# Performance work log

Hardware: AMD Instinct MI355X
Metric: run time of the kernel (lower is better)

Reference implementation:

```python
import jax, jax.numpy as jnp
import numpy as np

M, N, RANK = 4096, 4096, 64
LORA_ALPHA = 0.8
CODEBOOK_SCALE = 1.03  # E8P12 opt_scale; decompressed weights are divided by it


def fwht(x):
    """Normalized fast Walsh-Hadamard transform along the last axis (power-of-2 length).
    Matches matmul_hadU for power-of-2 dims (had_K is None, K=1)."""
    n = x.shape[-1]
    orig = x.shape
    x = x.reshape(-1, n)
    h = 1
    while h < n:
        x = x.reshape(-1, n // (2 * h), 2, h)
        a, b = x[:, :, 0, :], x[:, :, 1, :]
        x = jnp.stack([a + b, a - b], axis=2).reshape(-1, n)
        h *= 2
    return (x / jnp.sqrt(jnp.float32(n))).reshape(orig)


def decode_e8p(codes, grid):
    """E8P lattice codebook dequant (decompress_packed_e8p semantics).
    codes: int32 [M, N//8], one 16-bit codeword per 8-weight group.
    grid:  int32 [256] packed abs codebook; 8 nibbles per entry, nibble = 2*|w| in {1,3,5,7}.
    Bit layout: [0:8]=abs grid index, [8:15]=signs of first 7 coords,
    [15]=global +/-0.25 shift. 8th sign keeps the negative-sign count even."""
    abs_idx = codes & 0xFF
    sign_bits = (codes >> 8) & 0x7F
    shift_bit = (codes >> 15) & 1
    packed = grid[abs_idx]                                      # [M, N//8] int32
    nibs = (packed[..., None] >> (4 * jnp.arange(8))) & 0xF     # [M, N//8, 8]
    s7 = 1.0 - 2.0 * ((sign_bits[..., None] >> jnp.arange(7)) & 1).astype(jnp.float32)
    s8 = jnp.prod(s7, axis=-1, keepdims=True)                   # parity sign for 8th coord
    signs = jnp.concatenate([s7, s8], axis=-1)                  # [M, N//8, 8]
    delta = (2.0 * shift_bit.astype(jnp.float32) - 1.0)[..., None] * 0.25
    w = signs * (0.5 * nibs.astype(jnp.float32)) + delta
    return w.reshape(codes.shape[0], -1) / CODEBOOK_SCALE       # [M, N]


def build_W(Qidxs, grid, SU, SV, Wscale):
    W = decode_e8p(Qidxs, grid)   # [M, N]
    W = fwht(W)                   # Hadamard over in_features
    W = fwht(W.T).T               # Hadamard over out_features
    # per-channel sign/scale rescale; SV absorbs the global Wscale (SV *= Wscale)
    return W * (SV * Wscale)[:, None] * SU[None, :]


def setup_inputs() -> dict:
    key = jax.random.key(0)
    k1, k2, k3, k4, k5 = jax.random.split(key, 5)
    rng = np.random.default_rng(0)
    # packed abs codebook: 8 nibbles per int32, nibble = 2*|w| in {1,3,5,7}
    nibs = rng.integers(0, 4, size=(256, 8)).astype(np.int64) * 2 + 1
    grid = (nibs * (1 << (4 * np.arange(8)))).sum(axis=1).astype(np.int32)
    # one random 16-bit codeword per 8-weight group (int64 packing pre-split to int32)
    codes = rng.integers(0, 2 ** 16, size=(M, N // 8)).astype(np.int32)
    return {
        "input": jax.random.normal(k1, (1, 1024, N), dtype=jnp.float32),
        "SU": jnp.where(jax.random.uniform(k2, (N,)) < 0.5, -1.0, 1.0).astype(jnp.float32),
        "SV": jnp.where(jax.random.uniform(k3, (M,)) < 0.5, -1.0, 1.0).astype(jnp.float32),
        "Wscale": jnp.float32(0.02),
        "lora_A": jax.random.normal(k4, (M, RANK), dtype=jnp.float32) * 0.01,
        "lora_B": jax.random.normal(k5, (RANK, N), dtype=jnp.float32) * 0.01,
        "Qidxs": jnp.asarray(codes),
        "grid": jnp.asarray(grid),
    }


def reference(input, SU, SV, Wscale, lora_A, lora_B, Qidxs, grid):
    W = build_W(Qidxs, grid, SU, SV, Wscale)            # [M, N] dequantized weight
    out = jnp.einsum("bsn,mn->bsm", input, W)           # base quantized matmul
    lr = jnp.einsum("bsn,rn->bsr", input, lora_B)       # low-rank path
    out = out + LORA_ALPHA * jnp.einsum("bsr,mr->bsm", lr, lora_A)
    return out
```

## Files before the change

### kernel.cpp

```cpp
#include <hip/hip_runtime.h>
#include <hip/hip_bf16.h>

typedef unsigned short u16;
typedef float  floatx4 __attribute__((ext_vector_type(4)));
typedef short  bf16x8  __attribute__((ext_vector_type(8)));

#define GK 4224

__device__ __forceinline__ u16 f2bf_rne(float f) {
  union { float f; unsigned int u; } v; v.f = f;
  unsigned int r = v.u + 0x7FFFu + ((v.u >> 16) & 1u);
  return (u16)(r >> 16);
}

__device__ __forceinline__ void fwht4096_regs(float v[16], float* X, int w, int l) {
#pragma unroll
  for (int h = 1; h < 64; h <<= 1) {
#pragma unroll
    for (int k = 0; k < 16; ++k) {
      float o = __shfl_xor(v[k], h, 64);
      v[k] = (l & h) ? (o - v[k]) : (v[k] + o);
    }
  }
#pragma unroll
  for (int k = 0; k < 16; ++k) X[(w * 16 + k) * 64 + l] = v[k];
  __syncthreads();
  float s4 = (w & 1) ? -1.f : 1.f;
  float s5 = (w & 2) ? -1.f : 1.f;
#pragma unroll
  for (int k = 0; k < 16; ++k) {
    float x00 = X[(k     ) * 64 + l];
    float x01 = X[(k + 16) * 64 + l];
    float x10 = X[(k + 32) * 64 + l];
    float x11 = X[(k + 48) * 64 + l];
    v[k] = (x00 + s4 * x01) + s5 * (x10 + s4 * x11);
  }
#pragma unroll
  for (int h = 1; h < 16; h <<= 1) {
#pragma unroll
    for (int k = 0; k < 16; ++k) {
      if (!(k & h)) { float a = v[k], b = v[k ^ h]; v[k] = a + b; v[k ^ h] = a - b; }
    }
  }
}

__global__ void decode_kernel(const int* __restrict__ codes,
                              const int* __restrict__ grid,
                              u16* __restrict__ Wd) {
  __shared__ int sgrid[256];
  int t = threadIdx.x;
  sgrid[t] = grid[t & 255];
  __syncthreads();
  int idx = blockIdx.x * 256 + t;
  int c = codes[idx];
  int abs_idx   = c & 255;
  int sign_bits = (c >> 8) & 127;
  int dlt       = 2 * ((c >> 15) & 1) - 1;
  int packed    = sgrid[abs_idx];
  int par       = __popc(sign_bits) & 1;
  u16 w[8];
#pragma unroll
  for (int j = 0; j < 8; ++j) {
    int nib = (packed >> (4 * j)) & 15;
    int neg = (j < 7) ? ((sign_bits >> j) & 1) : par;
    int val = (neg ? -2 * nib : 2 * nib) + dlt;
    w[j] = f2bf_rne((float)val);
  }
  uint4 pk;
  pk.x = (unsigned)w[0] | ((unsigned)w[1] << 16);
  pk.y = (unsigned)w[2] | ((unsigned)w[3] << 16);
  pk.z = (unsigned)w[4] | ((unsigned)w[5] << 16);
  pk.w = (unsigned)w[6] | ((unsigned)w[7] << 16);
  int m = idx >> 9, g = idx & 511;
  ((uint4*)Wd)[(size_t)m * (GK / 8) + g] = pk;
}

__global__ __launch_bounds__(256) void prep_A_kernel(const float* __restrict__ loraA,
                                                     const float* __restrict__ SV,
                                                     const float* __restrict__ WscaleP,
                                                     u16* __restrict__ At) {
  __shared__ float X[4096];
  int r = blockIdx.x, t = threadIdx.x, l = t & 63, w = t >> 6;
  float v[16];
#pragma unroll
  for (int k = 0; k < 16; ++k) {
    int i = (w * 16 + k) * 64 + l;
    v[k] = loraA[(size_t)i * 64 + r] * SV[i];
  }
  fwht4096_regs(v, X, w, l);
  float factor = (0.8f * 263.68f / 4096.0f) / WscaleP[0];
#pragma unroll
  for (int k = 0; k < 16; ++k) {
    int i = (w * 16 + k) * 64 + l;
    At[(size_t)r * 4096 + i] = f2bf_rne(v[k] * factor);
  }
}

__global__ void transA_kernel(const u16* __restrict__ At, u16* __restrict__ Wd) {
  __shared__ u16 T[64][65];
  int m0 = blockIdx.x * 64, t = threadIdx.x;
  int c = t & 63, q = t >> 6;
#pragma unroll
  for (int j = 0; j < 16; ++j) {
    int r = q * 16 + j;
    T[r][c] = At[(size_t)r * 4096 + m0 + c];
  }
  __syncthreads();
#pragma unroll
  for (int j = 0; j < 16; ++j) {
    int m = q * 16 + j;
    Wd[(size_t)(m0 + m) * GK + 4096 + c] = T[c][m];
    Wd[(size_t)(m0 + m) * GK + 4160 + c] = 0;
  }
}

__global__ __launch_bounds__(256) void prep_B_kernel(const float* __restrict__ loraB,
                                                     const float* __restrict__ SU,
                                                     u16* __restrict__ Bh) {
  __shared__ float X[4096];
  int r = blockIdx.x, t = threadIdx.x, l = t & 63, w = t >> 6;
  float v[16];
#pragma unroll
  for (int k = 0; k < 16; ++k) {
    int i = (w * 16 + k) * 64 + l;
    v[k] = loraB[(size_t)r * 4096 + i] * SU[i];
  }
  fwht4096_regs(v, X, w, l);
#pragma unroll
  for (int k = 0; k < 16; ++k) {
    int i = (w * 16 + k) * 64 + l;
    Bh[(size_t)r * 4096 + i] = f2bf_rne(v[k] * 0.015625f);
  }
}

__global__ __launch_bounds__(256) void fwht_u_kernel(const float* __restrict__ x,
                                                     const float* __restrict__ SU,
                                                     u16* __restrict__ u) {
  __shared__ float X[4096];
  int s = blockIdx.x, t = threadIdx.x, l = t & 63, w = t >> 6;
  const float* xr = x + (size_t)s * 4096;
  float v[16];
#pragma unroll
  for (int k = 0; k < 16; ++k) {
    int i = (w * 16 + k) * 64 + l;
    v[k] = xr[i] * SU[i];
  }
  fwht4096_regs(v, X, w, l);
  u16* ur = u + (size_t)s * GK;
#pragma unroll
  for (int k = 0; k < 16; ++k) {
    int i = (w * 16 + k) * 64 + l;
    ur[i] = f2bf_rne(v[k] * 0.015625f);
  }
}

__device__ __forceinline__ void stage64(const u16* __restrict__ src, int rowBase,
                                        int kt, char* ldsBase, int wg, int l) {
#pragma unroll
  for (int it = 0; it < 4; ++it) {
    int ci  = it * 4 + wg;
    int row = ci * 8 + (l >> 3);
    int cg  = (l & 7) ^ ((l >> 3) & 7);
    const u16* gp = src + (size_t)(rowBase + row) * GK + kt + cg * 8;
    __builtin_amdgcn_global_load_lds(
        (const __attribute__((address_space(1))) void*)gp,
        (__attribute__((address_space(3))) void*)(ldsBase + ci * 1024), 16, 0, 0);
  }
}

__device__ __forceinline__ void stage64n(const u16* __restrict__ src,
                                         int kt, char* ldsBase, int wg, int l) {
#pragma unroll
  for (int it = 0; it < 2; ++it) {
    int ci  = it * 4 + wg;
    int row = ci * 8 + (l >> 3);
    int cg  = (l & 7) ^ ((l >> 3) & 7);
    const u16* gp = src + (size_t)row * 4096 + kt + cg * 8;
    __builtin_amdgcn_global_load_lds(
        (const __attribute__((address_space(1))) void*)gp,
        (__attribute__((address_space(3))) void*)(ldsBase + ci * 1024), 16, 0, 0);
  }
}

__global__ __launch_bounds__(256) void lr_gemm_kernel(
    const u16* __restrict__ U,
    const u16* __restrict__ Bh,
    float* __restrict__ P) {
  __shared__ char lds[49152];
  int t = threadIdx.x, w = t >> 6, l = t & 63;
  int s0 = blockIdx.x * 128, k0 = blockIdx.y * 1024;
  int lr16 = l & 15, lk = l >> 4;
  char* ldsA = lds;
  char* ldsB = lds + 32768;

  floatx4 acc[2][4];
#pragma unroll
  for (int i = 0; i < 2; ++i)
#pragma unroll
    for (int j = 0; j < 4; ++j) acc[i][j] = (floatx4){0.f, 0.f, 0.f, 0.f};

  const int NT = 16;
  stage64 (U,  s0, k0,      ldsA,         w, l);
  stage64n(Bh,     k0,      ldsB,         w, l);
  stage64 (U,  s0, k0 + 64, ldsA + 16384, w, l);
  stage64n(Bh,     k0 + 64, ldsB + 8192,  w, l);
  asm volatile("s_waitcnt vmcnt(6)" ::: "memory");
  __builtin_amdgcn_s_barrier();

  for (int i = 0; i < NT; ++i) {
    int buf = i & 1;
    const char* sAc = ldsA + buf * 16384;
    const char* sBc = ldsB + buf * 8192;
    bf16x8 a[2][2], b[4][2];
#pragma unroll
    for (int ii = 0; ii < 2; ++ii)
#pragma unroll
      for (int ks = 0; ks < 2; ++ks) {
        int row = w * 32 + ii * 16 + lr16;
        int kb  = ks * 64 + lk * 16;
        a[ii][ks] = *(const bf16x8*)(sAc + (row << 7) + (kb ^ ((row & 7) << 4)));
      }
#pragma unroll
    for (int jj = 0; jj < 4; ++jj)
#pragma unroll
      for (int ks = 0; ks < 2; ++ks) {
        int row = jj * 16 + lr16;
        int kb  = ks * 64 + lk * 16;
        b[jj][ks] = *(const bf16x8*)(sBc + (row << 7) + (kb ^ ((row & 7) << 4)));
      }
    asm volatile("s_waitcnt lgkmcnt(0)" ::: "memory");
    __builtin_amdgcn_sched_barrier(0);
    bool do_stage = (i + 2) < NT;
    if (do_stage) {
      __builtin_amdgcn_s_barrier();
      stage64 (U,  s0, k0 + (i + 2) * 64, ldsA + buf * 16384, w, l);
      stage64n(Bh,     k0 + (i + 2) * 64, ldsB + buf * 8192,  w, l);
    }
#pragma unroll
    for (int ks = 0; ks < 2; ++ks)
#pragma unroll
      for (int ii = 0; ii < 2; ++ii)
#pragma unroll
        for (int jj = 0; jj < 4; ++jj)
          acc[ii][jj] = __builtin_amdgcn_mfma_f32_16x16x32_bf16(
              a[ii][ks], b[jj][ks], acc[ii][jj], 0, 0, 0);
    if (i + 1 < NT) {
      if (do_stage) asm volatile("s_waitcnt vmcnt(6)" ::: "memory");
      else          asm volatile("s_waitcnt vmcnt(0)" ::: "memory");
      __builtin_amdgcn_s_barrier();
    }
  }
  float* Pb = P + (size_t)blockIdx.y * 65536;
#pragma unroll
  for (int ii = 0; ii < 2; ++ii)
#pragma unroll
    for (int jj = 0; jj < 4; ++jj) {
      int col  = jj * 16 + lr16;
      int rowb = s0 + w * 32 + ii * 16 + lk * 4;
#pragma unroll
      for (int q = 0; q < 4; ++q)
        Pb[(size_t)(rowb + q) * 64 + col] = acc[ii][jj][q];
    }
}

__global__ void lr_reduce_kernel(const float* __restrict__ P, u16* __restrict__ u) {
  int idx = blockIdx.x * 256 + threadIdx.x;
  float s = P[idx] + P[65536 + idx] + P[131072 + idx] + P[196608 + idx];
  int ss = idx >> 6, rr = idx & 63;
  u[(size_t)ss * GK + 4096 + rr] = f2bf_rne(s);
  u[(size_t)ss * GK + 4160 + rr] = 0;
}

__global__ __launch_bounds__(512) void gemm_kernel(
    const u16* __restrict__ A,
    const u16* __restrict__ B,
    float* __restrict__ Z) {
  __shared__ char lds[131072];
  int t = threadIdx.x, w = t >> 6, l = t & 63;
  int g = w >> 2, wg = w & 3;
  int m0 = blockIdx.x * 128, s0 = blockIdx.y * 128;
  int wm = wg >> 1, wn = wg & 1;
  int lr16 = l & 15, lk = l >> 4;
  char* gl = lds + g * 65536;

  floatx4 acc[4][4];
#pragma unroll
  for (int i = 0; i < 4; ++i)
#pragma unroll
    for (int j = 0; j < 4; ++j) acc[i][j] = (floatx4){0.f, 0.f, 0.f, 0.f};

  const int NT2 = 33;
  int kb0 = g * 2112;

  stage64(A, s0, kb0,      gl,         wg, l);
  stage64(B, m0, kb0,      gl + 32768, wg, l);
  stage64(A, s0, kb0 + 64, gl + 16384, wg, l);
  stage64(B, m0, kb0 + 64, gl + 49152, wg, l);
  asm volatile("s_waitcnt vmcnt(8)" ::: "memory");
  __builtin_amdgcn_s_barrier();

  for (int i = 0; i < NT2; ++i) {
    int buf = i & 1;
    const char* sAc = gl + buf * 16384;
    const char* sBc = gl + 32768 + buf * 16384;
    bf16x8 a[4][2], b[4][2];
#pragma unroll
    for (int ii = 0; ii < 4; ++ii)
#pragma unroll
      for (int ks = 0; ks < 2; ++ks) {
        int row = wm * 64 + ii * 16 + lr16;
        int kb  = ks * 64 + lk * 16;
        a[ii][ks] = *(const bf16x8*)(sAc + (row << 7) + (kb ^ ((row & 7) << 4)));
      }
#pragma unroll
    for (int jj = 0; jj < 4; ++jj)
#pragma unroll
      for (int ks = 0; ks < 2; ++ks) {
        int row = wn * 64 + jj * 16 + lr16;
        int kb  = ks * 64 + lk * 16;
        b[jj][ks] = *(const bf16x8*)(sBc + (row << 7) + (kb ^ ((row & 7) << 4)));
      }
    asm volatile("s_waitcnt lgkmcnt(0)" ::: "memory");
    __builtin_amdgcn_sched_barrier(0);
    bool do_stage = (i + 2) < NT2;
    if (do_stage) {
      __builtin_amdgcn_s_barrier();
      stage64(A, s0, kb0 + (i + 2) * 64, gl + buf * 16384, wg, l);
      stage64(B, m0, kb0 + (i + 2) * 64, gl + 32768 + buf * 16384, wg, l);
    }
#pragma unroll
    for (int ks = 0; ks < 2; ++ks)
#pragma unroll
      for (int ii = 0; ii < 4; ++ii)
#pragma unroll
        for (int jj = 0; jj < 4; ++jj)
          acc[ii][jj] = __builtin_amdgcn_mfma_f32_16x16x32_bf16(
              a[ii][ks], b[jj][ks], acc[ii][jj], 0, 0, 0);
    if (i + 1 < NT2) {
      if (do_stage) asm volatile("s_waitcnt vmcnt(8)" ::: "memory");
      else          asm volatile("s_waitcnt vmcnt(0)" ::: "memory");
      __builtin_amdgcn_s_barrier();
    }
  }

  __syncthreads();
  if (g == 1) {
#pragma unroll
    for (int ii = 0; ii < 4; ++ii)
#pragma unroll
      for (int jj = 0; jj < 4; ++jj)
        *(floatx4*)(lds + wg * 16384 + (ii * 4 + jj) * 1024 + l * 16) = acc[ii][jj];
  }
  __syncthreads();
  if (g == 0) {
#pragma unroll
    for (int ii = 0; ii < 4; ++ii)
#pragma unroll
      for (int jj = 0; jj < 4; ++jj) {
        floatx4 o = *(const floatx4*)(lds + wg * 16384 + (ii * 4 + jj) * 1024 + l * 16);
        acc[ii][jj] += o;
        int col  = m0 + wn * 64 + jj * 16 + lr16;
        int rowb = s0 + wm * 64 + ii * 16 + lk * 4;
#pragma unroll
        for (int q = 0; q < 4; ++q)
          Z[(size_t)(rowb + q) * 4096 + col] = acc[ii][jj][q];
      }
  }
}

__global__ __launch_bounds__(256) void final_kernel(const float* __restrict__ SV,
                                                    const float* __restrict__ WscaleP,
                                                    float* __restrict__ out) {
  __shared__ float X[4096];
  int s = blockIdx.x, t = threadIdx.x, l = t & 63, w = t >> 6;
  float* zr = out + (size_t)s * 4096;
  float v[16];
#pragma unroll
  for (int k = 0; k < 16; ++k) v[k] = zr[(w * 16 + k) * 64 + l];
  fwht4096_regs(v, X, w, l);
  float gscale = WscaleP[0] * (1.0f / 263.68f);
#pragma unroll
  for (int k = 0; k < 16; ++k) {
    int i = (w * 16 + k) * 64 + l;
    zr[i] = v[k] * gscale * SV[i];
  }
}

extern "C" void kernel_launch(void* const* d_in, const int* in_sizes, int n_in,
                              void* d_out, int out_size, void* d_ws, size_t ws_size,
                              hipStream_t stream) {
  const float* x      = (const float*)d_in[0];
  const float* SU     = (const float*)d_in[1];
  const float* SV     = (const float*)d_in[2];
  const float* Wscale = (const float*)d_in[3];
  const float* loraA  = (const float*)d_in[4];
  const float* loraB  = (const float*)d_in[5];
  const int*   Qidxs  = (const int*)d_in[6];
  const int*   grid   = (const int*)d_in[7];
  float* out = (float*)d_out;

  char* ws = (char*)d_ws;
  u16* Wd = (u16*)ws;
  u16* u  = (u16*)(ws + 34603008);
  u16* At = (u16*)(ws + 34603008 + 8650752);
  u16* Bh = At;
  float* P = (float*)(ws + 34603008 + 8650752 + 524288);
  float* z = out;

  decode_kernel<<<8192, 256, 0, stream>>>(Qidxs, grid, Wd);
  prep_A_kernel<<<64, 256, 0, stream>>>(loraA, SV, Wscale, At);
  transA_kernel<<<64, 256, 0, stream>>>(At, Wd);
  prep_B_kernel<<<64, 256, 0, stream>>>(loraB, SU, Bh);
  fwht_u_kernel<<<1024, 256, 0, stream>>>(x, SU, u);
  dim3 lg(8, 4);
  lr_gemm_kernel<<<lg, 256, 0, stream>>>(u, Bh, P);
  lr_reduce_kernel<<<256, 256, 0, stream>>>(P, u);
  dim3 gg(32, 8);
  gemm_kernel<<<gg, 512, 0, stream>>>(u, Wd, z);
  final_kernel<<<1024, 256, 0, stream>>>(SV, Wscale, out);
}
```

Measured before the change: 95.46 us.

## Split GEMM K across blocks with bf16 partials reduced in final kernel

The GEMM no longer splits K between two 4-wave groups inside one 512-thread block with an LDS reduction. It now launches a z-dimension of 2 blocks of 256 threads, and each block writes its K-half partial as bf16 into the output buffer. The final FWHT kernel sums the two bf16 partials before the transform. The main loop is also reordered to issue the first-half MFMAs before the barrier and staging, to overlap with loads. This gives more, smaller blocks with half the LDS and removes the in-block reduction, at the cost of bf16 rounding of the partial sums.

```diff
diff --git a/kernel.cpp b/kernel.cpp
--- a/kernel.cpp
+++ b/kernel.cpp
@@ -11,6 +11,10 @@
   union { float f; unsigned int u; } v; v.f = f;
   unsigned int r = v.u + 0x7FFFu + ((v.u >> 16) & 1u);
   return (u16)(r >> 16);
+}
+__device__ __forceinline__ float bf2f(u16 h) {
+  union { unsigned int u; float f; } v; v.u = ((unsigned int)h) << 16;
+  return v.f;
 }
 
 __device__ __forceinline__ void fwht4096_regs(float v[16], float* X, int w, int l) {
@@ -271,17 +275,15 @@
   u[(size_t)ss * GK + 4160 + rr] = 0;
 }
 
-__global__ __launch_bounds__(512) void gemm_kernel(
+__global__ __launch_bounds__(256) void gemm_kernel(
     const u16* __restrict__ A,
     const u16* __restrict__ B,
-    float* __restrict__ Z) {
-  __shared__ char lds[131072];
+    u16* __restrict__ zP) {
+  __shared__ char lds[65536];
   int t = threadIdx.x, w = t >> 6, l = t & 63;
-  int g = w >> 2, wg = w & 3;
-  int m0 = blockIdx.x * 128, s0 = blockIdx.y * 128;
-  int wm = wg >> 1, wn = wg & 1;
+  int m0 = blockIdx.x * 128, s0 = blockIdx.y * 128, g = blockIdx.z;
+  int wm = w >> 1, wn = w & 1;
   int lr16 = l & 15, lk = l >> 4;
-  char* gl = lds + g * 65536;
 
   floatx4 acc[4][4];
 #pragma unroll
@@ -289,83 +291,76 @@
 #pragma unroll
     for (int j = 0; j < 4; ++j) acc[i][j] = (floatx4){0.f, 0.f, 0.f, 0.f};
 
-  const int NT2 = 33;
+  const int NT = 33;
   int kb0 = g * 2112;
 
-  stage64(A, s0, kb0,      gl,         wg, l);
-  stage64(B, m0, kb0,      gl + 32768, wg, l);
-  stage64(A, s0, kb0 + 64, gl + 16384, wg, l);
-  stage64(B, m0, kb0 + 64, gl + 49152, wg, l);
+  stage64(A, s0, kb0,      lds,         w, l);
+  stage64(B, m0, kb0,      lds + 32768, w, l);
+  stage64(A, s0, kb0 + 64, lds + 16384, w, l);
+  stage64(B, m0, kb0 + 64, lds + 49152, w, l);
   asm volatile("s_waitcnt vmcnt(8)" ::: "memory");
   __builtin_amdgcn_s_barrier();
 
-  for (int i = 0; i < NT2; ++i) {
+  for (int i = 0; i < NT; ++i) {
     int buf = i & 1;
-    const char* sAc = gl + buf * 16384;
-    const char* sBc = gl + 32768 + buf * 16384;
+    const char* sAc = lds + buf * 16384;
+    const char* sBc = lds + 32768 + buf * 16384;
     bf16x8 a[4][2], b[4][2];
 #pragma unroll
+    for (int ii = 0; ii < 4; ++ii) {
+      int row = wm * 64 + ii * 16 + lr16;
+      a[ii][0] = *(const bf16x8*)(sAc + (row << 7) + ((lk * 16) ^ ((row & 7) << 4)));
+    }
+#pragma unroll
+    for (int jj = 0; jj < 4; ++jj) {
+      int row = wn * 64 + jj * 16 + lr16;
+      b[jj][0] = *(const bf16x8*)(sBc + (row << 7) + ((lk * 16) ^ ((row & 7) << 4)));
+    }
+#pragma unroll
+    for (int ii = 0; ii < 4; ++ii) {
+      int row = wm * 64 + ii * 16 + lr16;
+      a[ii][1] = *(const bf16x8*)(sAc + (row << 7) + ((64 + lk * 16) ^ ((row & 7) << 4)));
+    }
+#pragma unroll
+    for (int jj = 0; jj < 4; ++jj) {
+      int row = wn * 64 + jj * 16 + lr16;
+      b[jj][1] = *(const bf16x8*)(sBc + (row << 7) + ((64 + lk * 16) ^ ((row & 7) << 4)));
+    }
+#pragma unroll
     for (int ii = 0; ii < 4; ++ii)
 #pragma unroll
-      for (int ks = 0; ks < 2; ++ks) {
-        int row = wm * 64 + ii * 16 + lr16;
-        int kb  = ks * 64 + lk * 16;
-        a[ii][ks] = *(const bf16x8*)(sAc + (row << 7) + (kb ^ ((row & 7) << 4)));
-      }
-#pragma unroll
-    for (int jj = 0; jj < 4; ++jj)
-#pragma unroll
-      for (int ks = 0; ks < 2; ++ks) {
-        int row = wn * 64 + jj * 16 + lr16;
-        int kb  = ks * 64 + lk * 16;
-        b[jj][ks] = *(const bf16x8*)(sBc + (row << 7) + (kb ^ ((row & 7) << 4)));
-      }
+      for (int jj = 0; jj < 4; ++jj)
+        acc[ii][jj] = __builtin_amdgcn_mfma_f32_16x16x32_bf16(
+            a[ii][0], b[jj][0], acc[ii][jj], 0, 0, 0);
     asm volatile("s_waitcnt lgkmcnt(0)" ::: "memory");
-    __builtin_amdgcn_sched_barrier(0);
-    bool do_stage = (i + 2) < NT2;
+    __builtin_amdgcn_s_barrier();
+    bool do_stage = (i + 2) < NT;
     if (do_stage) {
-      __builtin_amdgcn_s_barrier();
-      stage64(A, s0, kb0 + (i + 2) * 64, gl + buf * 16384, wg, l);
-      stage64(B, m0, kb0 + (i + 2) * 64, gl + 32768 + buf * 16384, wg, l);
-    }
-#pragma unroll
-    for (int ks = 0; ks < 2; ++ks)
-#pragma unroll
-      for (int ii = 0; ii < 4; ++ii)
-#pragma unroll
-        for (int jj = 0; jj < 4; ++jj)
-          acc[ii][jj] = __builtin_amdgcn_mfma_f32_16x16x32_bf16(
-              a[ii][ks], b[jj][ks], acc[ii][jj], 0, 0, 0);
-    if (i + 1 < NT2) {
+      stage64(A, s0, kb0 + (i + 2) * 64, lds + buf * 16384, w, l);
+      stage64(B, m0, kb0 + (i + 2) * 64, lds + 32768 + buf * 16384, w, l);
+    }
+#pragma unroll
+    for (int ii = 0; ii < 4; ++ii)
+#pragma unroll
+      for (int jj = 0; jj < 4; ++jj)
+        acc[ii][jj] = __builtin_amdgcn_mfma_f32_16x16x32_bf16(
+            a[ii][1], b[jj][1], acc[ii][jj], 0, 0, 0);
+    if (i + 1 < NT) {
       if (do_stage) asm volatile("s_waitcnt vmcnt(8)" ::: "memory");
       else          asm volatile("s_waitcnt vmcnt(0)" ::: "memory");
       __builtin_amdgcn_s_barrier();
     }
   }
-
-  __syncthreads();
-  if (g == 1) {
-#pragma unroll
-    for (int ii = 0; ii < 4; ++ii)
-#pragma unroll
-      for (int jj = 0; jj < 4; ++jj)
-        *(floatx4*)(lds + wg * 16384 + (ii * 4 + jj) * 1024 + l * 16) = acc[ii][jj];
-  }
-  __syncthreads();
-  if (g == 0) {
-#pragma unroll
-    for (int ii = 0; ii < 4; ++ii)
-#pragma unroll
-      for (int jj = 0; jj < 4; ++jj) {
-        floatx4 o = *(const floatx4*)(lds + wg * 16384 + (ii * 4 + jj) * 1024 + l * 16);
-        acc[ii][jj] += o;
-        int col  = m0 + wn * 64 + jj * 16 + lr16;
-        int rowb = s0 + wm * 64 + ii * 16 + lk * 4;
-#pragma unroll
-        for (int q = 0; q < 4; ++q)
-          Z[(size_t)(rowb + q) * 4096 + col] = acc[ii][jj][q];
-      }
-  }
+#pragma unroll
+  for (int ii = 0; ii < 4; ++ii)
+#pragma unroll
+    for (int jj = 0; jj < 4; ++jj) {
+      int col  = m0 + wn * 64 + jj * 16 + lr16;
+      int rowb = s0 + wm * 64 + ii * 16 + lk * 4;
+#pragma unroll
+      for (int q = 0; q < 4; ++q)
+        zP[(size_t)(rowb + q) * 8192 + g * 4096 + col] = f2bf_rne(acc[ii][jj][q]);
+    }
 }
 
 __global__ __launch_bounds__(256) void final_kernel(const float* __restrict__ SV,
@@ -373,16 +368,20 @@
                                                     float* __restrict__ out) {
   __shared__ float X[4096];
   int s = blockIdx.x, t = threadIdx.x, l = t & 63, w = t >> 6;
-  float* zr = out + (size_t)s * 4096;
+  const u16* zr = (const u16*)out + (size_t)s * 8192;
   float v[16];
 #pragma unroll
-  for (int k = 0; k < 16; ++k) v[k] = zr[(w * 16 + k) * 64 + l];
+  for (int k = 0; k < 16; ++k) {
+    int i = (w * 16 + k) * 64 + l;
+    v[k] = bf2f(zr[i]) + bf2f(zr[4096 + i]);
+  }
   fwht4096_regs(v, X, w, l);
   float gscale = WscaleP[0] * (1.0f / 263.68f);
-#pragma unroll
-  for (int k = 0; k < 16; ++k) {
-    int i = (w * 16 + k) * 64 + l;
-    zr[i] = v[k] * gscale * SV[i];
+  float* orow = out + (size_t)s * 4096;
+#pragma unroll
+  for (int k = 0; k < 16; ++k) {
+    int i = (w * 16 + k) * 64 + l;
+    orow[i] = v[k] * gscale * SV[i];
   }
 }
 
@@ -405,7 +404,7 @@
   u16* At = (u16*)(ws + 34603008 + 8650752);
   u16* Bh = At;
   float* P = (float*)(ws + 34603008 + 8650752 + 524288);
-  float* z = out;
+  u16* zP = (u16*)out;
 
   decode_kernel<<<8192, 256, 0, stream>>>(Qidxs, grid, Wd);
   prep_A_kernel<<<64, 256, 0, stream>>>(loraA, SV, Wscale, At);
@@ -415,7 +414,7 @@
   dim3 lg(8, 4);
   lr_gemm_kernel<<<lg, 256, 0, stream>>>(u, Bh, P);
   lr_reduce_kernel<<<256, 256, 0, stream>>>(P, u);
-  dim3 gg(32, 8);
-  gemm_kernel<<<gg, 512, 0, stream>>>(u, Wd, z);
+  dim3 gg(32, 8, 2);
+  gemm_kernel<<<gg, 256, 0, stream>>>(u, Wd, zP);
   final_kernel<<<1024, 256, 0, stream>>>(SV, Wscale, out);
 }
```

Result: slower. 98.51 us (+3.2%).
